# Kernel optimization log

Measured on AMD Instinct MI355X. Metric: run time of the kernel, lower is better.

Reference implementation:

```python
import jax, jax.numpy as jnp
import numpy as np

C_CURV = 1.0          # Poincare ball curvature
EPS = 1e-5
MAX_NORM = (1.0 - 1e-4) / np.sqrt(C_CURV)


def _artanh(x):
    x = jnp.clip(x, -1.0 + 1e-5, 1.0 - 1e-5)
    return 0.5 * (jnp.log1p(x) - jnp.log1p(-x))


def _expmap0(v):
    # v: [N,C,H,W]; norm over channel dim per spatial location
    n = jnp.maximum(jnp.linalg.norm(v, axis=1, keepdims=True), EPS)
    sc = np.sqrt(C_CURV)
    return jnp.tanh(sc * n) * v / (sc * n)


def _logmap0(y):
    n = jnp.maximum(jnp.linalg.norm(y, axis=1, keepdims=True), EPS)
    sc = np.sqrt(C_CURV)
    return _artanh(sc * n) * y / (sc * n)


def _project(y):
    # clamp back inside the ball
    n = jnp.maximum(jnp.linalg.norm(y, axis=1, keepdims=True), EPS)
    return jnp.where(n > MAX_NORM, y * (MAX_NORM / n), y)


def _conv3x3(u, w, b):
    y = jax.lax.conv_general_dilated(u, w, window_strides=(1, 1),
                                     padding=((1, 1), (1, 1)),
                                     dimension_numbers=('NCHW', 'OIHW', 'NCHW'))
    return y + b[None, :, None, None]


def _hconv(x, w, b):
    # HConvolution2d: tangent-space conv around origin
    return _project(_expmap0(_conv3x3(_logmap0(x), w, b)))


def _hbn(x, gamma, beta):
    # HBatchNorm2d: Euclidean BN in the tangent space at the origin (training stats)
    u = _logmap0(x)
    m = u.mean(axis=(0, 2, 3), keepdims=True)
    v = u.var(axis=(0, 2, 3), keepdims=True)
    u = (u - m) / jnp.sqrt(v + 1e-5)
    u = u * gamma[None, :, None, None] + beta[None, :, None, None]
    return _project(_expmap0(u))


def _hrelu(x):
    return _project(_expmap0(jax.nn.relu(_logmap0(x))))


def setup_inputs() -> dict:
    key = jax.random.key(0)
    ks = jax.random.split(key, 8)
    N, Cin, Cmid, Cout, H, W = 8, 32, 32, 32, 256, 256
    # input point on the Poincare ball
    x = _project(_expmap0(0.1 * jax.random.normal(ks[0], (N, Cin, H, W), jnp.float32)))
    fan1 = Cin * 9
    fan2 = Cmid * 9
    w1 = jax.random.normal(ks[1], (Cmid, Cin, 3, 3), jnp.float32) / np.sqrt(fan1)
    b1 = jnp.zeros((Cmid,), jnp.float32)
    g1 = jnp.ones((Cmid,), jnp.float32)
    beta1 = jnp.zeros((Cmid,), jnp.float32)
    w2 = jax.random.normal(ks[2], (Cout, Cmid, 3, 3), jnp.float32) / np.sqrt(fan2)
    b2 = jnp.zeros((Cout,), jnp.float32)
    g2 = jnp.ones((Cout,), jnp.float32)
    beta2 = jnp.zeros((Cout,), jnp.float32)
    return {"x": x, "w1": w1, "b1": b1, "g1": g1, "beta1": beta1,
            "w2": w2, "b2": b2, "g2": g2, "beta2": beta2}


def reference(x, w1, b1, g1, beta1, w2, b2, g2, beta2):
    out = _hconv(x, w1, b1)
    out = _hbn(out, g1, beta1)
    out = _hrelu(out)
    out = _hconv(out, w2, b2)
    out = _hbn(out, g2, beta2)
    out = _hrelu(out)
    return out
```

## Files before the change

### kernel.cpp

```cpp
#include <hip/hip_runtime.h>
#include <math.h>

#define HWDIM 256
#define CH 32
#define NB 8
#define TILE 16
#define NLOC (NB*HWDIM*HWDIM)
#define R_CLAMP 4.9517189f
#define MAXN 0.9999f
#define BN_EPS 1e-5f
#define EPSF 1e-5f
#define NBLK 2048
#define OST 264

typedef __attribute__((ext_vector_type(8))) _Float16 half8;
typedef __attribute__((ext_vector_type(4))) _Float16 half4;
typedef __attribute__((ext_vector_type(4))) float floatx4;

__device__ __forceinline__ float artanh_c(float n) {
    float t = fminf(n, 1.0f - 1e-5f);
    return 0.5f * (log1pf(t) - log1pf(-t));
}

__global__ __launch_bounds__(256) void wprep_kernel(
    const float* __restrict__ w1, const float* __restrict__ w2,
    _Float16* __restrict__ wp1, _Float16* __restrict__ wp2)
{
    int idx = blockIdx.x * 256 + threadIdx.x;
    if (idx >= 2*CH*CH*9) return;
    int s = idx >= CH*CH*9;
    int id = idx - s*(CH*CH*9);
    const float* w = s ? w2 : w1;
    _Float16* wp = s ? wp2 : wp1;
    int j  = id & 7;
    int r  = id >> 3;
    int co = r & 31;
    int og = r >> 5;
    int g  = og & 3;
    int o  = og >> 2;
    int ci = g*8 + j;
    wp[id] = (_Float16)w[(co*CH + ci)*9 + o];
}

template<int STAGE>
__global__ __launch_bounds__(256) void conv_mfma_kernel(
    const void* __restrict__ srcv,
    const _Float16* __restrict__ wp,
    const float* __restrict__ bias,
    const float* __restrict__ scsh,
    _Float16* __restrict__ dst,
    float* __restrict__ partials)
{
    __shared__ _Float16 ah[10368];
    __shared__ float red[4][64];

    const int tid = threadIdx.x;
    const int flat = blockIdx.x;
    const int bz = flat & 7;
    const int t  = flat >> 3;
    const int by = t >> 4, bx = t & 15;
    const int h0 = by*TILE - 1, w0 = bx*TILE - 1;

    for (int loc = tid; loc < 324; loc += 256) {
        int y = loc / 18, x = loc - y*18;
        int gh = h0 + y, gw = w0 + x;
        if (gh < 0 || gh >= HWDIM || gw < 0 || gw >= HWDIM) {
            half8 z = {0,0,0,0,0,0,0,0};
            #pragma unroll
            for (int g = 0; g < 4; g++) *(half8*)(ah + ((y*4+g)*18 + x)*8) = z;
            continue;
        }
        float v[CH]; float n2 = 0.f;
        if (STAGE == 1) {
            const float* p = (const float*)srcv + ((size_t)bz*CH << 16) + gh*HWDIM + gw;
            #pragma unroll
            for (int c = 0; c < CH; c++) { float t0 = p[(size_t)c << 16]; v[c] = t0; n2 = fmaf(t0, t0, n2); }
            float n = fmaxf(sqrtf(n2), EPSF);
            float f = artanh_c(n) / n;
            #pragma unroll
            for (int c = 0; c < CH; c++) v[c] *= f;
        } else {
            const _Float16* p = (const _Float16*)srcv + (((size_t)bz << 16) + gh*HWDIM + gw)*CH;
            half8 raw[4];
            #pragma unroll
            for (int k = 0; k < 4; k++) raw[k] = *(const half8*)(p + 8*k);
            #pragma unroll
            for (int c = 0; c < CH; c++) {
                float t0 = fmaf((float)raw[c>>3][c&7], scsh[c], scsh[CH + c]);
                v[c] = t0; n2 = fmaf(t0, t0, n2);
            }
            float n = sqrtf(n2);
            float f = (n > R_CLAMP) ? (R_CLAMP / n) : 1.0f;
            #pragma unroll
            for (int c = 0; c < CH; c++) v[c] = fmaxf(v[c]*f, 0.0f);
        }
        #pragma unroll
        for (int g = 0; g < 4; g++) {
            half8 hv;
            #pragma unroll
            for (int j = 0; j < 8; j++) hv[j] = (_Float16)v[g*8 + j];
            *(half8*)(ah + ((y*4+g)*18 + x)*8) = hv;
        }
    }
    __syncthreads();

    const int lane = tid & 63, wave = tid >> 6;
    const int xx = lane & 15, q = lane >> 4;

    floatx4 acc[4][2];
    #pragma unroll
    for (int i = 0; i < 4; i++) {
        acc[i][0] = (floatx4){0.f,0.f,0.f,0.f};
        acc[i][1] = (floatx4){0.f,0.f,0.f,0.f};
    }

    #pragma unroll
    for (int dx = 0; dx < 3; dx++) {
        half8 af[6];
        #pragma unroll
        for (int yy = 0; yy < 6; yy++)
            af[yy] = *(const half8*)(ah + (((wave*4+yy)*4 + q)*18 + xx + dx)*8);
        #pragma unroll
        for (int dy = 0; dy < 3; dy++) {
            const int o = dy*3 + dx;
            const _Float16* wb = wp + (size_t)((o*4 + q)*32)*8;
            half8 wf0 = *(const half8*)(wb + xx*8);
            half8 wf1 = *(const half8*)(wb + (xx+16)*8);
            #pragma unroll
            for (int i = 0; i < 4; i++) {
                acc[i][0] = __builtin_amdgcn_mfma_f32_16x16x32_f16(wf0, af[i+dy], acc[i][0], 0,0,0);
                acc[i][1] = __builtin_amdgcn_mfma_f32_16x16x32_f16(wf1, af[i+dy], acc[i][1], 0,0,0);
            }
        }
    }

    float bs[8];
    #pragma unroll
    for (int r = 0; r < 4; r++) { bs[r] = bias[q*4+r]; bs[4+r] = bias[q*4+r+16]; }
    float sv[8], qv[8];
    #pragma unroll
    for (int k = 0; k < 8; k++) { sv[k] = 0.f; qv[k] = 0.f; }

    _Float16* dp = dst + (((size_t)bz << 16) + (size_t)(by*TILE)*HWDIM + bx*TILE + xx)*CH + q*4;

    #pragma unroll
    for (int i = 0; i < 4; i++) {
        float n2 = 0.f;
        #pragma unroll
        for (int r = 0; r < 4; r++) {
            acc[i][0][r] += bs[r];
            acc[i][1][r] += bs[4+r];
            n2 = fmaf(acc[i][0][r], acc[i][0][r], n2);
            n2 = fmaf(acc[i][1][r], acc[i][1][r], n2);
        }
        n2 += __shfl_xor(n2, 16, 64);
        n2 += __shfl_xor(n2, 32, 64);
        float nn = sqrtf(n2);
        float f = (nn > R_CLAMP) ? (R_CLAMP/nn) : 1.0f;
        half4 o0, o1;
        #pragma unroll
        for (int r = 0; r < 4; r++) {
            float a0 = acc[i][0][r] * f;
            float a1 = acc[i][1][r] * f;
            sv[r]   += a0; qv[r]   = fmaf(a0, a0, qv[r]);
            sv[4+r] += a1; qv[4+r] = fmaf(a1, a1, qv[4+r]);
            o0[r] = (_Float16)a0; o1[r] = (_Float16)a1;
        }
        _Float16* a = dp + (size_t)(wave*4 + i)*HWDIM*CH;
        *(half4*)(a)      = o0;
        *(half4*)(a + 16) = o1;
    }

    #pragma unroll
    for (int k = 0; k < 8; k++) {
        #pragma unroll
        for (int m = 1; m < 16; m <<= 1) {
            sv[k] += __shfl_xor(sv[k], m, 64);
            qv[k] += __shfl_xor(qv[k], m, 64);
        }
    }
    if (xx == 0) {
        #pragma unroll
        for (int r = 0; r < 4; r++) {
            red[wave][q*4+r]        = sv[r];
            red[wave][16 + q*4+r]   = sv[4+r];
            red[wave][32 + q*4+r]   = qv[r];
            red[wave][48 + q*4+r]   = qv[4+r];
        }
    }
    __syncthreads();
    if (tid < 64) {
        float s = red[0][tid] + red[1][tid] + red[2][tid] + red[3][tid];
        partials[(size_t)tid*NBLK + flat] = s;
    }
}

__global__ __launch_bounds__(256) void finalize_kernel(
    const float* __restrict__ partials,
    const float* __restrict__ g, const float* __restrict__ beta,
    float* __restrict__ scsh)
{
    __shared__ float ss[256], sq[256];
    const int c = blockIdx.x;
    const int tid = threadIdx.x;
    float s = 0.f, q = 0.f;
    for (int b = tid; b < NBLK; b += 256) {
        s += partials[(size_t)c*NBLK + b];
        q += partials[(size_t)(CH + c)*NBLK + b];
    }
    ss[tid] = s; sq[tid] = q;
    __syncthreads();
    for (int st = 128; st > 0; st >>= 1) {
        if (tid < st) { ss[tid] += ss[tid+st]; sq[tid] += sq[tid+st]; }
        __syncthreads();
    }
    if (tid == 0) {
        const float NS = (float)NLOC;
        float mean = ss[0] / NS;
        float var = fmaxf(sq[0] / NS - mean*mean, 0.0f);
        float sc = g[c] / sqrtf(var + BN_EPS);
        scsh[c] = sc;
        scsh[CH + c] = beta[c] - mean*sc;
    }
}

__global__ __launch_bounds__(256) void out_kernel(
    const _Float16* __restrict__ t4c, const float* __restrict__ scsh,
    float* __restrict__ out)
{
    __shared__ float outb[16*OST];
    const int w = threadIdx.x;
    const int h = blockIdx.x, n = blockIdx.y;
    const _Float16* p = t4c + (((size_t)n << 16) + (size_t)h*HWDIM + w)*CH;
    half8 raw[4];
    #pragma unroll
    for (int k = 0; k < 4; k++) raw[k] = *(const half8*)(p + 8*k);
    float u[CH]; float n2 = 0.f;
    #pragma unroll
    for (int c = 0; c < CH; c++) {
        float t = fmaf((float)raw[c>>3][c&7], scsh[c], scsh[CH+c]);
        u[c] = t; n2 = fmaf(t, t, n2);
    }
    float nn = sqrtf(n2);
    float f = (nn > R_CLAMP) ? (R_CLAMP/nn) : 1.0f;
    float r2 = 0.f;
    #pragma unroll
    for (int c = 0; c < CH; c++) { float r = fmaxf(u[c]*f, 0.0f); u[c] = r; r2 = fmaf(r, r, r2); }
    float rn = fmaxf(sqrtf(r2), EPSF);
    float s = fminf(tanhf(rn), MAXN) / rn;
    #pragma unroll
    for (int c = 0; c < CH; c++) u[c] *= s;

    #pragma unroll
    for (int hf = 0; hf < 2; hf++) {
        if (hf) __syncthreads();
        #pragma unroll
        for (int c = 0; c < 16; c++) outb[c*OST + w] = u[hf*16 + c];
        __syncthreads();
        int co = threadIdx.x >> 4, seg = threadIdx.x & 15;
        const float* row = outb + co*OST + seg*16;
        float* gp = out + ((size_t)(n*CH + hf*16 + co) << 16) + (size_t)h*HWDIM + seg*16;
        #pragma unroll
        for (int k = 0; k < 4; k++) *(floatx4*)(gp + 4*k) = *(const floatx4*)(row + 4*k);
    }
}

extern "C" void kernel_launch(void* const* d_in, const int* in_sizes, int n_in,
                              void* d_out, int out_size, void* d_ws, size_t ws_size,
                              hipStream_t stream)
{
    const float* x   = (const float*)d_in[0];
    const float* w1  = (const float*)d_in[1];
    const float* b1  = (const float*)d_in[2];
    const float* g1  = (const float*)d_in[3];
    const float* be1 = (const float*)d_in[4];
    const float* w2  = (const float*)d_in[5];
    const float* b2  = (const float*)d_in[6];
    const float* g2  = (const float*)d_in[7];
    const float* be2 = (const float*)d_in[8];
    float* outf = (float*)d_out;

    char* ws = (char*)d_ws;
    _Float16* wp1   = (_Float16*)ws;
    _Float16* wp2   = wp1 + 9216;
    float* partials = (float*)(ws + 36864);
    float* scsh1    = (float*)(ws + 36864 + 524288);
    float* scsh2    = scsh1 + 64;
    _Float16* t1c   = (_Float16*)(scsh2 + 64);
    _Float16* t4c   = t1c + (size_t)NLOC*CH;

    wprep_kernel<<<72, 256, 0, stream>>>(w1, w2, wp1, wp2);

    conv_mfma_kernel<1><<<NBLK, 256, 0, stream>>>(x, wp1, b1, scsh1, t1c, partials);
    finalize_kernel<<<32, 256, 0, stream>>>(partials, g1, be1, scsh1);
    conv_mfma_kernel<2><<<NBLK, 256, 0, stream>>>(t1c, wp2, b2, scsh1, t4c, partials);
    finalize_kernel<<<32, 256, 0, stream>>>(partials, g2, be2, scsh2);
    out_kernel<<<dim3(HWDIM, NB), 256, 0, stream>>>(t4c, scsh2, outf);
}
```

Baseline: 203.5 us.

## Make conv blocks persistent over 4 tiles with register prefetch of next halo

The conv kernel now launches 512 blocks of 512 threads, and each block walks 4 horizontally adjacent 16x16 tiles. The next tile's halo is loaded into registers while MFMAs run on the current one, and the 8 waves each take 2 rows. This is meant to hide global load latency behind compute and cut the number of BN partials to reduce. It also swaps in fast log and divide intrinsics for artanh and the clamps, and raises wave priority around the MFMA loop. The costs are higher register pressure from the prefetch buffers, fewer and larger blocks, and slightly lower precision from the fast math.

```diff
diff --git a/kernel.cpp b/kernel.cpp
--- a/kernel.cpp
+++ b/kernel.cpp
@@ -10,16 +10,17 @@
 #define MAXN 0.9999f
 #define BN_EPS 1e-5f
 #define EPSF 1e-5f
-#define NBLK 2048
+#define GRIDC 512
+#define TPB 4
 #define OST 264
 
 typedef __attribute__((ext_vector_type(8))) _Float16 half8;
 typedef __attribute__((ext_vector_type(4))) _Float16 half4;
 typedef __attribute__((ext_vector_type(4))) float floatx4;
 
-__device__ __forceinline__ float artanh_c(float n) {
+__device__ __forceinline__ float artanh_fast(float n) {
     float t = fminf(n, 1.0f - 1e-5f);
-    return 0.5f * (log1pf(t) - log1pf(-t));
+    return 0.5f * __logf(__fdividef(1.0f + t, 1.0f - t));
 }
 
 __global__ __launch_bounds__(256) void wprep_kernel(
@@ -43,7 +44,7 @@
 }
 
 template<int STAGE>
-__global__ __launch_bounds__(256) void conv_mfma_kernel(
+__global__ __launch_bounds__(512, 4) void conv_mfma_kernel(
     const void* __restrict__ srcv,
     const _Float16* __restrict__ wp,
     const float* __restrict__ bias,
@@ -52,45 +53,70 @@
     float* __restrict__ partials)
 {
     __shared__ _Float16 ah[10368];
-    __shared__ float red[4][64];
+    __shared__ float red[8][64];
 
     const int tid = threadIdx.x;
-    const int flat = blockIdx.x;
-    const int bz = flat & 7;
-    const int t  = flat >> 3;
-    const int by = t >> 4, bx = t & 15;
-    const int h0 = by*TILE - 1, w0 = bx*TILE - 1;
-
-    for (int loc = tid; loc < 324; loc += 256) {
-        int y = loc / 18, x = loc - y*18;
-        int gh = h0 + y, gw = w0 + x;
-        if (gh < 0 || gh >= HWDIM || gw < 0 || gw >= HWDIM) {
+    const int b   = blockIdx.x;
+    const int bz  = b & 7;
+    const int tb  = b >> 3;
+    const int by  = tb >> 2;
+    const int bx0 = (tb & 3) * TPB;
+    const int h0  = by*TILE - 1;
+
+    const int lane = tid & 63, wave = tid >> 6;
+    const int xx = lane & 15, q = lane >> 4;
+
+    const bool sact = (tid < 324);
+    int sy = 0, sx = 0;
+    if (sact) { sy = tid / 18; sx = tid - sy*18; }
+    const int gh = h0 + sy;
+    const bool rowok = sact && (gh >= 0) && (gh < HWDIM);
+
+    float  pf[CH];
+    half8  praw[4];
+    bool   inb = false;
+
+    auto PREFETCH = [&](int j) {
+        if (!sact) return;
+        const int gw = bx0*TILE + j*TILE - 1 + sx;
+        inb = rowok && (gw >= 0) && (gw < HWDIM);
+        if (!inb) return;
+        if (STAGE == 1) {
+            const float* p = (const float*)srcv + ((size_t)bz*CH << 16) + gh*HWDIM + gw;
+            #pragma unroll
+            for (int c = 0; c < CH; c++) pf[c] = p[(size_t)c << 16];
+        } else {
+            const _Float16* p = (const _Float16*)srcv + (((size_t)bz << 16) + gh*HWDIM + gw)*CH;
+            #pragma unroll
+            for (int k = 0; k < 4; k++) praw[k] = *(const half8*)(p + 8*k);
+        }
+    };
+
+    auto TRANSFORM = [&]() {
+        if (!sact) return;
+        _Float16* base = ah + ((sy*4)*18 + sx)*8;
+        if (!inb) {
             half8 z = {0,0,0,0,0,0,0,0};
             #pragma unroll
-            for (int g = 0; g < 4; g++) *(half8*)(ah + ((y*4+g)*18 + x)*8) = z;
-            continue;
+            for (int g = 0; g < 4; g++) *(half8*)(base + g*18*8) = z;
+            return;
         }
         float v[CH]; float n2 = 0.f;
         if (STAGE == 1) {
-            const float* p = (const float*)srcv + ((size_t)bz*CH << 16) + gh*HWDIM + gw;
-            #pragma unroll
-            for (int c = 0; c < CH; c++) { float t0 = p[(size_t)c << 16]; v[c] = t0; n2 = fmaf(t0, t0, n2); }
+            #pragma unroll
+            for (int c = 0; c < CH; c++) { float t0 = pf[c]; v[c] = t0; n2 = fmaf(t0, t0, n2); }
             float n = fmaxf(sqrtf(n2), EPSF);
-            float f = artanh_c(n) / n;
+            float f = __fdividef(artanh_fast(n), n);
             #pragma unroll
             for (int c = 0; c < CH; c++) v[c] *= f;
         } else {
-            const _Float16* p = (const _Float16*)srcv + (((size_t)bz << 16) + gh*HWDIM + gw)*CH;
-            half8 raw[4];
-            #pragma unroll
-            for (int k = 0; k < 4; k++) raw[k] = *(const half8*)(p + 8*k);
             #pragma unroll
             for (int c = 0; c < CH; c++) {
-                float t0 = fmaf((float)raw[c>>3][c&7], scsh[c], scsh[CH + c]);
+                float t0 = fmaf((float)praw[c>>3][c&7], scsh[c], scsh[CH + c]);
                 v[c] = t0; n2 = fmaf(t0, t0, n2);
             }
             float n = sqrtf(n2);
-            float f = (n > R_CLAMP) ? (R_CLAMP / n) : 1.0f;
+            float f = (n > R_CLAMP) ? __fdividef(R_CLAMP, n) : 1.0f;
             #pragma unroll
             for (int c = 0; c < CH; c++) v[c] = fmaxf(v[c]*f, 0.0f);
         }
@@ -98,41 +124,10 @@
         for (int g = 0; g < 4; g++) {
             half8 hv;
             #pragma unroll
-            for (int j = 0; j < 8; j++) hv[j] = (_Float16)v[g*8 + j];
-            *(half8*)(ah + ((y*4+g)*18 + x)*8) = hv;
-        }
-    }
-    __syncthreads();
-
-    const int lane = tid & 63, wave = tid >> 6;
-    const int xx = lane & 15, q = lane >> 4;
-
-    floatx4 acc[4][2];
-    #pragma unroll
-    for (int i = 0; i < 4; i++) {
-        acc[i][0] = (floatx4){0.f,0.f,0.f,0.f};
-        acc[i][1] = (floatx4){0.f,0.f,0.f,0.f};
-    }
-
-    #pragma unroll
-    for (int dx = 0; dx < 3; dx++) {
-        half8 af[6];
-        #pragma unroll
-        for (int yy = 0; yy < 6; yy++)
-            af[yy] = *(const half8*)(ah + (((wave*4+yy)*4 + q)*18 + xx + dx)*8);
-        #pragma unroll
-        for (int dy = 0; dy < 3; dy++) {
-            const int o = dy*3 + dx;
-            const _Float16* wb = wp + (size_t)((o*4 + q)*32)*8;
-            half8 wf0 = *(const half8*)(wb + xx*8);
-            half8 wf1 = *(const half8*)(wb + (xx+16)*8);
-            #pragma unroll
-            for (int i = 0; i < 4; i++) {
-                acc[i][0] = __builtin_amdgcn_mfma_f32_16x16x32_f16(wf0, af[i+dy], acc[i][0], 0,0,0);
-                acc[i][1] = __builtin_amdgcn_mfma_f32_16x16x32_f16(wf1, af[i+dy], acc[i][1], 0,0,0);
-            }
-        }
-    }
+            for (int j2 = 0; j2 < 8; j2++) hv[j2] = (_Float16)v[g*8 + j2];
+            *(half8*)(base + g*18*8) = hv;
+        }
+    };
 
     float bs[8];
     #pragma unroll
@@ -141,34 +136,72 @@
     #pragma unroll
     for (int k = 0; k < 8; k++) { sv[k] = 0.f; qv[k] = 0.f; }
 
-    _Float16* dp = dst + (((size_t)bz << 16) + (size_t)(by*TILE)*HWDIM + bx*TILE + xx)*CH + q*4;
-
-    #pragma unroll
-    for (int i = 0; i < 4; i++) {
-        float n2 = 0.f;
-        #pragma unroll
-        for (int r = 0; r < 4; r++) {
-            acc[i][0][r] += bs[r];
-            acc[i][1][r] += bs[4+r];
-            n2 = fmaf(acc[i][0][r], acc[i][0][r], n2);
-            n2 = fmaf(acc[i][1][r], acc[i][1][r], n2);
-        }
-        n2 += __shfl_xor(n2, 16, 64);
-        n2 += __shfl_xor(n2, 32, 64);
-        float nn = sqrtf(n2);
-        float f = (nn > R_CLAMP) ? (R_CLAMP/nn) : 1.0f;
-        half4 o0, o1;
-        #pragma unroll
-        for (int r = 0; r < 4; r++) {
-            float a0 = acc[i][0][r] * f;
-            float a1 = acc[i][1][r] * f;
-            sv[r]   += a0; qv[r]   = fmaf(a0, a0, qv[r]);
-            sv[4+r] += a1; qv[4+r] = fmaf(a1, a1, qv[4+r]);
-            o0[r] = (_Float16)a0; o1[r] = (_Float16)a1;
-        }
-        _Float16* a = dp + (size_t)(wave*4 + i)*HWDIM*CH;
-        *(half4*)(a)      = o0;
-        *(half4*)(a + 16) = o1;
+    PREFETCH(0);
+
+    #pragma unroll 1
+    for (int j = 0; j < TPB; j++) {
+        TRANSFORM();
+        __syncthreads();
+        if (j + 1 < TPB) PREFETCH(j + 1);
+
+        floatx4 acc[2][2];
+        #pragma unroll
+        for (int i = 0; i < 2; i++) {
+            acc[i][0] = (floatx4){0.f,0.f,0.f,0.f};
+            acc[i][1] = (floatx4){0.f,0.f,0.f,0.f};
+        }
+
+        __builtin_amdgcn_s_setprio(1);
+        #pragma unroll
+        for (int dx = 0; dx < 3; dx++) {
+            half8 af[4];
+            #pragma unroll
+            for (int yy = 0; yy < 4; yy++)
+                af[yy] = *(const half8*)(ah + (((wave*2+yy)*4 + q)*18 + xx + dx)*8);
+            #pragma unroll
+            for (int dy = 0; dy < 3; dy++) {
+                const int o = dy*3 + dx;
+                const _Float16* wb = wp + (size_t)((o*4 + q)*32)*8;
+                half8 wf0 = *(const half8*)(wb + xx*8);
+                half8 wf1 = *(const half8*)(wb + (xx+16)*8);
+                #pragma unroll
+                for (int i = 0; i < 2; i++) {
+                    acc[i][0] = __builtin_amdgcn_mfma_f32_16x16x32_f16(wf0, af[i+dy], acc[i][0], 0,0,0);
+                    acc[i][1] = __builtin_amdgcn_mfma_f32_16x16x32_f16(wf1, af[i+dy], acc[i][1], 0,0,0);
+                }
+            }
+        }
+        __builtin_amdgcn_s_setprio(0);
+
+        _Float16* dp = dst + (((size_t)bz << 16) + (size_t)(by*TILE)*HWDIM + (bx0 + j)*TILE + xx)*CH + q*4;
+        #pragma unroll
+        for (int i = 0; i < 2; i++) {
+            float n2 = 0.f;
+            #pragma unroll
+            for (int r = 0; r < 4; r++) {
+                acc[i][0][r] += bs[r];
+                acc[i][1][r] += bs[4+r];
+                n2 = fmaf(acc[i][0][r], acc[i][0][r], n2);
+                n2 = fmaf(acc[i][1][r], acc[i][1][r], n2);
+            }
+            n2 += __shfl_xor(n2, 16, 64);
+            n2 += __shfl_xor(n2, 32, 64);
+            float nn = sqrtf(n2);
+            float f = (nn > R_CLAMP) ? __fdividef(R_CLAMP, nn) : 1.0f;
+            half4 o0, o1;
+            #pragma unroll
+            for (int r = 0; r < 4; r++) {
+                float a0 = acc[i][0][r] * f;
+                float a1 = acc[i][1][r] * f;
+                sv[r]   += a0; qv[r]   = fmaf(a0, a0, qv[r]);
+                sv[4+r] += a1; qv[4+r] = fmaf(a1, a1, qv[4+r]);
+                o0[r] = (_Float16)a0; o1[r] = (_Float16)a1;
+            }
+            _Float16* a = dp + (size_t)(wave*2 + i)*HWDIM*CH;
+            *(half4*)(a)      = o0;
+            *(half4*)(a + 16) = o1;
+        }
+        __syncthreads();
     }
 
     #pragma unroll
@@ -190,8 +223,10 @@
     }
     __syncthreads();
     if (tid < 64) {
-        float s = red[0][tid] + red[1][tid] + red[2][tid] + red[3][tid];
-        partials[(size_t)tid*NBLK + flat] = s;
+        float s = 0.f;
+        #pragma unroll
+        for (int w = 0; w < 8; w++) s += red[w][tid];
+        partials[(size_t)tid*GRIDC + b] = s;
     }
 }
 
@@ -204,9 +239,9 @@
     const int c = blockIdx.x;
     const int tid = threadIdx.x;
     float s = 0.f, q = 0.f;
-    for (int b = tid; b < NBLK; b += 256) {
-        s += partials[(size_t)c*NBLK + b];
-        q += partials[(size_t)(CH + c)*NBLK + b];
+    for (int b = tid; b < GRIDC; b += 256) {
+        s += partials[(size_t)c*GRIDC + b];
+        q += partials[(size_t)(CH + c)*GRIDC + b];
     }
     ss[tid] = s; sq[tid] = q;
     __syncthreads();
@@ -291,9 +326,9 @@
 
     wprep_kernel<<<72, 256, 0, stream>>>(w1, w2, wp1, wp2);
 
-    conv_mfma_kernel<1><<<NBLK, 256, 0, stream>>>(x, wp1, b1, scsh1, t1c, partials);
+    conv_mfma_kernel<1><<<GRIDC, 512, 0, stream>>>(x, wp1, b1, scsh1, t1c, partials);
     finalize_kernel<<<32, 256, 0, stream>>>(partials, g1, be1, scsh1);
-    conv_mfma_kernel<2><<<NBLK, 256, 0, stream>>>(t1c, wp2, b2, scsh1, t4c, partials);
+    conv_mfma_kernel<2><<<GRIDC, 512, 0, stream>>>(t1c, wp2, b2, scsh1, t4c, partials);
     finalize_kernel<<<32, 256, 0, stream>>>(partials, g2, be2, scsh2);
     out_kernel<<<dim3(HWDIM, NB), 256, 0, stream>>>(t4c, scsh2, outf);
 }
```

Result: slower. 318.6 us (+56.5%).
